# Optimization experiments

Hardware: AMD Instinct MI355X
Metric: run time of the kernel (lower is better)

## Reference

```python
import jax, jax.numpy as jnp
import numpy as np

B, N, D, H, C = 16, 196, 768, 3072, 10

def setup_inputs() -> dict:
    key = jax.random.key(0)
    ks = jax.random.split(key, 8)
    s1 = 1.0 / np.sqrt(D)
    s2 = 1.0 / np.sqrt(H)
    return {
        "x": jax.random.normal(ks[0], (B, N, D), jnp.float32),
        "y": jax.random.randint(ks[1], (B,), 0, C),
        "W1": jax.random.normal(ks[2], (H, D), jnp.float32) * s1,
        "b1": jax.random.normal(ks[3], (H,), jnp.float32) * 0.01,
        "W2": jax.random.normal(ks[4], (D, H), jnp.float32) * s2,
        "b2": jax.random.normal(ks[5], (D,), jnp.float32) * 0.01,
        "mask_fc1": jax.random.uniform(ks[6], (C, H, D), jnp.float32),
        "mask_fc2": jax.random.uniform(ks[7], (C, D, H), jnp.float32),
    }

def reference(x, y, W1, b1, W2, b2, mask_fc1, mask_fc2):
    # per-sample masked weights: [B, out, in]
    Wm1 = W1[None, :, :] * mask_fc1[y]          # [B, H, D]
    h = jnp.einsum('bni,boi->bno', x, Wm1) + b1  # [B, N, H]
    h = jax.nn.gelu(h, approximate=False)        # act (drop1/norm are identity)
    Wm2 = W2[None, :, :] * mask_fc2[y]           # [B, D, H]
    out = jnp.einsum('bni,boi->bno', h, Wm2) + b2  # [B, N, D]
    return out
```

## Files before the change

### kernel.cpp

```cpp
#include <hip/hip_runtime.h>
#include <hip/hip_bf16.h>
#include <math.h>

#define B_ 16
#define N_ 196
#define D_ 768
#define H_ 3072
#define C_ 10

typedef __attribute__((ext_vector_type(8))) short bf16x8;
typedef __attribute__((ext_vector_type(4))) float f32x4;

__device__ __forceinline__ ushort f2bu(float f) {
    union { float f; unsigned u; } c; c.f = f;
    unsigned u = c.u;
    unsigned r = (u + 0x7FFFu + ((u >> 16) & 1u)) >> 16;
    return (ushort)r;
}

__device__ __forceinline__ void gl_lds16(const ushort* g, ushort* l) {
    __builtin_amdgcn_global_load_lds(
        (const __attribute__((address_space(1))) void*)g,
        (__attribute__((address_space(3))) void*)l, 16, 0, 0);
}

__global__ void scan_y(const int* __restrict__ y, int* __restrict__ used) {
    if (threadIdx.x < C_) used[threadIdx.x] = 0;
    __syncthreads();
    if (threadIdx.x < B_) used[y[threadIdx.x]] = 1;
}

__global__ __launch_bounds__(256) void build_wm(
    const float* __restrict__ W, const float* __restrict__ mask,
    const int* __restrict__ used, ushort* __restrict__ outw)
{
    const int c = blockIdx.y;
    if (!used[c]) return;
    const long n = (long)H_ * D_;
    const long i = ((long)blockIdx.x * 256 + threadIdx.x) * 8;
    const float4* wp = reinterpret_cast<const float4*>(W + i);
    const float4* mp = reinterpret_cast<const float4*>(mask + c * n + i);
    float4 w0 = wp[0], w1 = wp[1], m0 = mp[0], m1 = mp[1];
    ushort t[8] = { f2bu(w0.x*m0.x), f2bu(w0.y*m0.y), f2bu(w0.z*m0.z), f2bu(w0.w*m0.w),
                    f2bu(w1.x*m1.x), f2bu(w1.y*m1.y), f2bu(w1.z*m1.z), f2bu(w1.w*m1.w) };
    *reinterpret_cast<uint4*>(outw + c * n + i) = *reinterpret_cast<const uint4*>(t);
}

__global__ __launch_bounds__(256) void cvt_x(const float* __restrict__ x,
                                             ushort* __restrict__ xb) {
    const int i = blockIdx.x * 256 + threadIdx.x;
    const float4* src = reinterpret_cast<const float4*>(x) + (size_t)i * 2;
    float4 a = src[0], b = src[1];
    ushort t[8] = { f2bu(a.x), f2bu(a.y), f2bu(a.z), f2bu(a.w),
                    f2bu(b.x), f2bu(b.y), f2bu(b.z), f2bu(b.w) };
    reinterpret_cast<uint4*>(xb)[i] = *reinterpret_cast<const uint4*>(t);
}

template<int EPI>
__global__ __launch_bounds__(256) void mgemm(
    const ushort* __restrict__ A0, const ushort* __restrict__ Wm,
    const int* __restrict__ y, const float* __restrict__ bias1,
    ushort* __restrict__ hout, float* __restrict__ pout)
{
    constexpr int K = (EPI == 0) ? D_ : H_;
    __shared__ ushort As[128][64];
    __shared__ ushort Bs[128][64];

    const int ot = blockIdx.x;
    const int mt = blockIdx.y;
    const int z  = blockIdx.z;
    const int b  = (EPI == 0) ? z : (z >> 2);
    const int sk = (EPI == 0) ? 0 : (z & 3);
    const int cls = y[b];
    const int tid = threadIdx.x, lane = tid & 63, wid = tid >> 6;
    const int wm = wid >> 1, wn = wid & 1;
    const int fr = lane & 15, fq = lane >> 4;
    const int lr = lane >> 3, le = (lane & 7) * 8;

    const ushort* Ab = A0 + (long)b * N_ * K;
    const ushort* Bb = Wm + (long)cls * ((long)H_ * D_) + (long)(ot * 128) * K;

    f32x4 acc[4][4] = {};
    const int kt0 = (EPI == 0) ? 0 : sk * 12;

    #pragma unroll
    for (int t = 0; t < 12; ++t) {
        const int k0 = (kt0 + t) * 64;
        #pragma unroll
        for (int i = 0; i < 4; ++i) {
            const int r = wid * 32 + i * 8;
            const int gm = min(mt * 128 + r + lr, N_ - 1);
            gl_lds16(Ab + (long)gm * K + k0 + le, &As[r][0]);
        }
        #pragma unroll
        for (int i = 0; i < 4; ++i) {
            const int r = wid * 32 + i * 8;
            gl_lds16(Bb + (long)(r + lr) * K + k0 + le, &Bs[r][0]);
        }
        __syncthreads();
        #pragma unroll
        for (int kk = 0; kk < 64; kk += 32) {
            bf16x8 af[4], bf[4];
            #pragma unroll
            for (int i = 0; i < 4; ++i)
                af[i] = *reinterpret_cast<const bf16x8*>(&As[wm*64 + i*16 + fr][kk + fq*8]);
            #pragma unroll
            for (int j = 0; j < 4; ++j)
                bf[j] = *reinterpret_cast<const bf16x8*>(&Bs[wn*64 + j*16 + fr][kk + fq*8]);
            #pragma unroll
            for (int i = 0; i < 4; ++i)
                #pragma unroll
                for (int j = 0; j < 4; ++j)
                    acc[i][j] = __builtin_amdgcn_mfma_f32_16x16x32_bf16(af[i], bf[j], acc[i][j], 0, 0, 0);
        }
        __syncthreads();
    }

    if (EPI == 0) {
        #pragma unroll
        for (int j = 0; j < 4; ++j) {
            const int o = ot*128 + wn*64 + j*16 + fr;
            const float bias = bias1[o];
            #pragma unroll
            for (int i = 0; i < 4; ++i) {
                #pragma unroll
                for (int e = 0; e < 4; ++e) {
                    const int m = mt*128 + wm*64 + i*16 + fq*4 + e;
                    if (m < N_) {
                        float v = acc[i][j][e] + bias;
                        v = 0.5f * v * (1.0f + erff(v * 0.70710678118654752f));
                        hout[((long)b * N_ + m) * H_ + o] = f2bu(v);
                    }
                }
            }
        }
    } else {
        float* op = pout + (size_t)sk * (size_t)(B_ * N_ * D_);
        #pragma unroll
        for (int j = 0; j < 4; ++j) {
            const int o = ot*128 + wn*64 + j*16 + fr;
            #pragma unroll
            for (int i = 0; i < 4; ++i) {
                #pragma unroll
                for (int e = 0; e < 4; ++e) {
                    const int m = mt*128 + wm*64 + i*16 + fq*4 + e;
                    if (m < N_)
                        op[((long)b * N_ + m) * D_ + o] = acc[i][j][e];
                }
            }
        }
    }
}

__global__ __launch_bounds__(256) void reduce_k(const float* __restrict__ part,
                                                const float* __restrict__ b2,
                                                float* __restrict__ out, int SK)
{
    const int i = blockIdx.x * 256 + threadIdx.x;
    const int stride4 = B_ * N_ * D_ / 4;
    float4 s = reinterpret_cast<const float4*>(part)[i];
    for (int k = 1; k < SK; ++k) {
        float4 p = reinterpret_cast<const float4*>(part)[(size_t)k * stride4 + i];
        s.x += p.x; s.y += p.y; s.z += p.z; s.w += p.w;
    }
    const int ob = (i % (D_ / 4)) * 4;
    float4 bias = *reinterpret_cast<const float4*>(b2 + ob);
    s.x += bias.x; s.y += bias.y; s.z += bias.z; s.w += bias.w;
    reinterpret_cast<float4*>(out)[i] = s;
}

__global__ __launch_bounds__(256) void fb_gemm1(
    const float* __restrict__ x, const int* __restrict__ y,
    const float* __restrict__ W1, const float* __restrict__ b1,
    const float* __restrict__ mask1, ushort* __restrict__ h)
{
    __shared__ ushort As[128][72];
    __shared__ ushort Bs[64][72];
    const int ot = blockIdx.x, mt = blockIdx.y, b = blockIdx.z;
    const int cls = y[b];
    const int tid = threadIdx.x, lane = tid & 63, wid = tid >> 6;
    const int wm = wid >> 1, wn = wid & 1;
    const int fr = lane & 15, fq = lane >> 4;
    const int sr = tid >> 2, sc = (tid & 3) * 16;
    f32x4 acc[4][2] = {};
    const long xbase = ((long)b * N_) * D_;
    const long wbase = (long)(ot * 64) * D_;
    const long mbase = ((long)cls * H_ + ot * 64) * D_;
    for (int kt = 0; kt < D_ / 64; ++kt) {
        const int k0 = kt * 64 + sc;
        #pragma unroll
        for (int half = 0; half < 2; ++half) {
            const int r = sr + half * 64;
            const int m = mt * 128 + r;
            ushort tmp[16];
            if (m < N_) {
                const float4* src = reinterpret_cast<const float4*>(x + xbase + (long)m * D_ + k0);
                #pragma unroll
                for (int j = 0; j < 4; ++j) {
                    float4 v = src[j];
                    tmp[4*j+0]=f2bu(v.x); tmp[4*j+1]=f2bu(v.y); tmp[4*j+2]=f2bu(v.z); tmp[4*j+3]=f2bu(v.w);
                }
            } else { for (int j = 0; j < 16; ++j) tmp[j] = 0; }
            *reinterpret_cast<uint4*>(&As[r][sc])   = *reinterpret_cast<const uint4*>(&tmp[0]);
            *reinterpret_cast<uint4*>(&As[r][sc+8]) = *reinterpret_cast<const uint4*>(&tmp[8]);
        }
        {
            const float4* wsrc = reinterpret_cast<const float4*>(W1 + wbase + (long)sr * D_ + k0);
            const float4* msrc = reinterpret_cast<const float4*>(mask1 + mbase + (long)sr * D_ + k0);
            ushort tmp[16];
            #pragma unroll
            for (int j = 0; j < 4; ++j) {
                float4 wv = wsrc[j], mv = msrc[j];
                tmp[4*j+0]=f2bu(wv.x*mv.x); tmp[4*j+1]=f2bu(wv.y*mv.y);
                tmp[4*j+2]=f2bu(wv.z*mv.z); tmp[4*j+3]=f2bu(wv.w*mv.w);
            }
            *reinterpret_cast<uint4*>(&Bs[sr][sc])   = *reinterpret_cast<const uint4*>(&tmp[0]);
            *reinterpret_cast<uint4*>(&Bs[sr][sc+8]) = *reinterpret_cast<const uint4*>(&tmp[8]);
        }
        __syncthreads();
        #pragma unroll
        for (int kk = 0; kk < 64; kk += 32) {
            bf16x8 af[4], bf[2];
            #pragma unroll
            for (int i = 0; i < 4; ++i) af[i] = *reinterpret_cast<const bf16x8*>(&As[wm*64+i*16+fr][kk+fq*8]);
            #pragma unroll
            for (int j = 0; j < 2; ++j) bf[j] = *reinterpret_cast<const bf16x8*>(&Bs[wn*32+j*16+fr][kk+fq*8]);
            #pragma unroll
            for (int i = 0; i < 4; ++i)
                #pragma unroll
                for (int j = 0; j < 2; ++j)
                    acc[i][j] = __builtin_amdgcn_mfma_f32_16x16x32_bf16(af[i], bf[j], acc[i][j], 0, 0, 0);
        }
        __syncthreads();
    }
    #pragma unroll
    for (int j = 0; j < 2; ++j) {
        const int o = ot*64 + wn*32 + j*16 + fr;
        const float bias = b1[o];
        #pragma unroll
        for (int i = 0; i < 4; ++i)
            #pragma unroll
            for (int e = 0; e < 4; ++e) {
                const int m = mt*128 + wm*64 + i*16 + fq*4 + e;
                if (m < N_) {
                    float v = acc[i][j][e] + bias;
                    v = 0.5f * v * (1.0f + erff(v * 0.70710678118654752f));
                    h[(((long)b * N_) + m) * H_ + o] = f2bu(v);
                }
            }
    }
}

__global__ __launch_bounds__(256) void fb_gemm2(
    const ushort* __restrict__ h, const int* __restrict__ y,
    const float* __restrict__ W2, const float* __restrict__ b2,
    const float* __restrict__ mask2, float* __restrict__ dst,
    int split, int nkt, int add_bias)
{
    __shared__ ushort As[128][72];
    __shared__ ushort Bs[64][72];
    const int ot = blockIdx.x, mt = blockIdx.y, z = blockIdx.z;
    const int b = z / split, sk = z - b * split;
    const int cls = y[b];
    const int tid = threadIdx.x, lane = tid & 63, wid = tid >> 6;
    const int wm = wid >> 1, wn = wid & 1;
    const int fr = lane & 15, fq = lane >> 4;
    const int sr = tid >> 2, sc = (tid & 3) * 16;
    f32x4 acc[4][2] = {};
    const long hbase = ((long)b * N_) * H_;
    const long wbase = (long)(ot * 64) * H_;
    const long mbase = ((long)cls * D_ + ot * 64) * H_;
    const int kt0 = sk * nkt;
    for (int kt = kt0; kt < kt0 + nkt; ++kt) {
        const int k0 = kt * 64 + sc;
        #pragma unroll
        for (int half = 0; half < 2; ++half) {
            const int r = sr + half * 64;
            const int m = mt * 128 + r;
            if (m < N_) {
                const uint4* src = reinterpret_cast<const uint4*>(h + hbase + (long)m * H_ + k0);
                *reinterpret_cast<uint4*>(&As[r][sc])   = src[0];
                *reinterpret_cast<uint4*>(&As[r][sc+8]) = src[1];
            } else {
                uint4 z4 = {0u,0u,0u,0u};
                *reinterpret_cast<uint4*>(&As[r][sc])   = z4;
                *reinterpret_cast<uint4*>(&As[r][sc+8]) = z4;
            }
        }
        {
            const float4* wsrc = reinterpret_cast<const float4*>(W2 + wbase + (long)sr * H_ + k0);
            const float4* msrc = reinterpret_cast<const float4*>(mask2 + mbase + (long)sr * H_ + k0);
            ushort tmp[16];
            #pragma unroll
            for (int j = 0; j < 4; ++j) {
                float4 wv = wsrc[j], mv = msrc[j];
                tmp[4*j+0]=f2bu(wv.x*mv.x); tmp[4*j+1]=f2bu(wv.y*mv.y);
                tmp[4*j+2]=f2bu(wv.z*mv.z); tmp[4*j+3]=f2bu(wv.w*mv.w);
            }
            *reinterpret_cast<uint4*>(&Bs[sr][sc])   = *reinterpret_cast<const uint4*>(&tmp[0]);
            *reinterpret_cast<uint4*>(&Bs[sr][sc+8]) = *reinterpret_cast<const uint4*>(&tmp[8]);
        }
        __syncthreads();
        #pragma unroll
        for (int kk = 0; kk < 64; kk += 32) {
            bf16x8 af[4], bf[2];
            #pragma unroll
            for (int i = 0; i < 4; ++i) af[i] = *reinterpret_cast<const bf16x8*>(&As[wm*64+i*16+fr][kk+fq*8]);
            #pragma unroll
            for (int j = 0; j < 2; ++j) bf[j] = *reinterpret_cast<const bf16x8*>(&Bs[wn*32+j*16+fr][kk+fq*8]);
            #pragma unroll
            for (int i = 0; i < 4; ++i)
                #pragma unroll
                for (int j = 0; j < 2; ++j)
                    acc[i][j] = __builtin_amdgcn_mfma_f32_16x16x32_bf16(af[i], bf[j], acc[i][j], 0, 0, 0);
        }
        __syncthreads();
    }
    float* op = dst + (size_t)sk * (size_t)(B_ * N_ * D_);
    #pragma unroll
    for (int j = 0; j < 2; ++j) {
        const int o = ot*64 + wn*32 + j*16 + fr;
        const float bias = add_bias ? b2[o] : 0.0f;
        #pragma unroll
        for (int i = 0; i < 4; ++i)
            #pragma unroll
            for (int e = 0; e < 4; ++e) {
                const int m = mt*128 + wm*64 + i*16 + fq*4 + e;
                if (m < N_) op[(((long)b * N_) + m) * D_ + o] = acc[i][j][e] + bias;
            }
    }
}

extern "C" void kernel_launch(void* const* d_in, const int* in_sizes, int n_in,
                              void* d_out, int out_size, void* d_ws, size_t ws_size,
                              hipStream_t stream) {
    const float* x  = (const float*)d_in[0];
    const int*   y  = (const int*)d_in[1];
    const float* W1 = (const float*)d_in[2];
    const float* b1 = (const float*)d_in[3];
    const float* W2 = (const float*)d_in[4];
    const float* b2 = (const float*)d_in[5];
    const float* m1 = (const float*)d_in[6];
    const float* m2 = (const float*)d_in[7];
    float* out = (float*)d_out;

    const size_t hB  = (size_t)B_ * N_ * H_ * 2;
    const size_t oB  = (size_t)B_ * N_ * D_ * 4;
    const size_t xB  = (size_t)B_ * N_ * D_ * 2;
    const size_t wmB = (size_t)C_ * H_ * D_ * 2;

    const size_t off_part = hB;
    const size_t off_xb   = hB + 4 * oB;
    const size_t off_used = off_xb + xB;
    const size_t off_wm1  = off_used + 256;
    const size_t off_wm2  = off_wm1 + wmB;
    const size_t need     = off_wm2 + wmB;

    ushort* h = (ushort*)d_ws;

    if (ws_size >= need) {
        float*  part = (float*)((char*)d_ws + off_part);
        ushort* xb   = (ushort*)((char*)d_ws + off_xb);
        int*    used = (int*)((char*)d_ws + off_used);
        ushort* wm1  = (ushort*)((char*)d_ws + off_wm1);
        ushort* wm2  = (ushort*)((char*)d_ws + off_wm2);

        scan_y<<<1, 64, 0, stream>>>(y, used);
        build_wm<<<dim3(1152, C_), 256, 0, stream>>>(W1, m1, used, wm1);
        build_wm<<<dim3(1152, C_), 256, 0, stream>>>(W2, m2, used, wm2);
        cvt_x<<<1176, 256, 0, stream>>>(x, xb);
        mgemm<0><<<dim3(24, 2, 16), 256, 0, stream>>>(xb, wm1, y, b1, h, nullptr);
        mgemm<1><<<dim3(6, 2, 64), 256, 0, stream>>>(h, wm2, y, nullptr, nullptr, part);
        reduce_k<<<(B_ * N_ * D_ / 4) / 256, 256, 0, stream>>>(part, b2, out, 4);
    } else {
        int SK = 0;
        if      (ws_size >= hB + 4 * oB) SK = 4;
        else if (ws_size >= hB + 2 * oB) SK = 2;
        float* part = (float*)((char*)d_ws + hB);
        dim3 g1(H_ / 64, 2, B_);
        fb_gemm1<<<g1, 256, 0, stream>>>(x, y, W1, b1, m1, h);
        if (SK) {
            dim3 g2(D_ / 64, 2, B_ * SK);
            fb_gemm2<<<g2, 256, 0, stream>>>(h, y, W2, b2, m2, part, SK, 48 / SK, 0);
            reduce_k<<<(B_ * N_ * D_ / 4) / 256, 256, 0, stream>>>(part, b2, out, SK);
        } else {
            dim3 g2(D_ / 64, 2, B_);
            fb_gemm2<<<g2, 256, 0, stream>>>(h, y, W2, b2, m2, out, 1, 48, 1);
        }
    }
}
```

Baseline: 144.3 us.

## Fuse prep kernels and overlap fc1 GEMM with fc2 weight masking

Merges the scan, masked-W1 build and x conversion into one launch, then co-schedules the first GEMM with the masked-W2 build in a single heterogeneous grid so the W2 build overlaps GEMM1. Each block now checks y itself instead of reading a separate used-flag array. Activations are padded to 256 rows per batch, which removes the row clamp and the bounds checks in the GEMM loads and epilogue. In exchange GEMM1 computes GELU on padded garbage rows, and the combined grid mixes compute-bound and memory-bound blocks whose scheduling order is not controlled.

After: 142.1 us. Within noise of the previous version (-1.5%).

```diff
diff --git a/kernel.cpp b/kernel.cpp
--- a/kernel.cpp
+++ b/kernel.cpp
@@ -7,6 +7,7 @@
 #define D_ 768
 #define H_ 3072
 #define C_ 10
+#define MPAD 256
 
 typedef __attribute__((ext_vector_type(8))) short bf16x8;
 typedef __attribute__((ext_vector_type(4))) float f32x4;
@@ -24,60 +25,43 @@
         (__attribute__((address_space(3))) void*)l, 16, 0, 0);
 }
 
-__global__ void scan_y(const int* __restrict__ y, int* __restrict__ used) {
-    if (threadIdx.x < C_) used[threadIdx.x] = 0;
-    __syncthreads();
-    if (threadIdx.x < B_) used[y[threadIdx.x]] = 1;
-}
-
-__global__ __launch_bounds__(256) void build_wm(
+__device__ __forceinline__ void build_wm_chunk(
     const float* __restrict__ W, const float* __restrict__ mask,
-    const int* __restrict__ used, ushort* __restrict__ outw)
-{
-    const int c = blockIdx.y;
-    if (!used[c]) return;
+    const int* __restrict__ y, ushort* __restrict__ outw,
+    int c, int chunk)
+{
+    bool used = false;
+    #pragma unroll
+    for (int t = 0; t < B_; ++t) used |= (y[t] == c);
+    if (!used) return;
     const long n = (long)H_ * D_;
-    const long i = ((long)blockIdx.x * 256 + threadIdx.x) * 8;
+    const long i = (long)chunk * 2048 + threadIdx.x * 8;
     const float4* wp = reinterpret_cast<const float4*>(W + i);
     const float4* mp = reinterpret_cast<const float4*>(mask + c * n + i);
     float4 w0 = wp[0], w1 = wp[1], m0 = mp[0], m1 = mp[1];
-    ushort t[8] = { f2bu(w0.x*m0.x), f2bu(w0.y*m0.y), f2bu(w0.z*m0.z), f2bu(w0.w*m0.w),
-                    f2bu(w1.x*m1.x), f2bu(w1.y*m1.y), f2bu(w1.z*m1.z), f2bu(w1.w*m1.w) };
-    *reinterpret_cast<uint4*>(outw + c * n + i) = *reinterpret_cast<const uint4*>(t);
-}
-
-__global__ __launch_bounds__(256) void cvt_x(const float* __restrict__ x,
-                                             ushort* __restrict__ xb) {
-    const int i = blockIdx.x * 256 + threadIdx.x;
-    const float4* src = reinterpret_cast<const float4*>(x) + (size_t)i * 2;
-    float4 a = src[0], b = src[1];
-    ushort t[8] = { f2bu(a.x), f2bu(a.y), f2bu(a.z), f2bu(a.w),
-                    f2bu(b.x), f2bu(b.y), f2bu(b.z), f2bu(b.w) };
-    reinterpret_cast<uint4*>(xb)[i] = *reinterpret_cast<const uint4*>(t);
+    ushort t8[8] = { f2bu(w0.x*m0.x), f2bu(w0.y*m0.y), f2bu(w0.z*m0.z), f2bu(w0.w*m0.w),
+                     f2bu(w1.x*m1.x), f2bu(w1.y*m1.y), f2bu(w1.z*m1.z), f2bu(w1.w*m1.w) };
+    *reinterpret_cast<uint4*>(outw + c * n + i) = *reinterpret_cast<const uint4*>(t8);
 }
 
 template<int EPI>
-__global__ __launch_bounds__(256) void mgemm(
+__device__ __forceinline__ void gemm_core(
     const ushort* __restrict__ A0, const ushort* __restrict__ Wm,
     const int* __restrict__ y, const float* __restrict__ bias1,
-    ushort* __restrict__ hout, float* __restrict__ pout)
+    ushort* __restrict__ hout, float* __restrict__ pout,
+    int ot, int mt, int b, int sk)
 {
     constexpr int K = (EPI == 0) ? D_ : H_;
     __shared__ ushort As[128][64];
     __shared__ ushort Bs[128][64];
 
-    const int ot = blockIdx.x;
-    const int mt = blockIdx.y;
-    const int z  = blockIdx.z;
-    const int b  = (EPI == 0) ? z : (z >> 2);
-    const int sk = (EPI == 0) ? 0 : (z & 3);
     const int cls = y[b];
     const int tid = threadIdx.x, lane = tid & 63, wid = tid >> 6;
     const int wm = wid >> 1, wn = wid & 1;
     const int fr = lane & 15, fq = lane >> 4;
     const int lr = lane >> 3, le = (lane & 7) * 8;
 
-    const ushort* Ab = A0 + (long)b * N_ * K;
+    const ushort* Ab = A0 + ((long)b * MPAD + mt * 128) * K;
     const ushort* Bb = Wm + (long)cls * ((long)H_ * D_) + (long)(ot * 128) * K;
 
     f32x4 acc[4][4] = {};
@@ -89,8 +73,7 @@
         #pragma unroll
         for (int i = 0; i < 4; ++i) {
             const int r = wid * 32 + i * 8;
-            const int gm = min(mt * 128 + r + lr, N_ - 1);
-            gl_lds16(Ab + (long)gm * K + k0 + le, &As[r][0]);
+            gl_lds16(Ab + (long)(r + lr) * K + k0 + le, &As[r][0]);
         }
         #pragma unroll
         for (int i = 0; i < 4; ++i) {
@@ -126,11 +109,9 @@
                 #pragma unroll
                 for (int e = 0; e < 4; ++e) {
                     const int m = mt*128 + wm*64 + i*16 + fq*4 + e;
-                    if (m < N_) {
-                        float v = acc[i][j][e] + bias;
-                        v = 0.5f * v * (1.0f + erff(v * 0.70710678118654752f));
-                        hout[((long)b * N_ + m) * H_ + o] = f2bu(v);
-                    }
+                    float v = acc[i][j][e] + bias;
+                    v = 0.5f * v * (1.0f + erff(v * 0.70710678118654752f));
+                    hout[((long)b * MPAD + m) * H_ + o] = f2bu(v);
                 }
             }
         }
@@ -150,6 +131,53 @@
             }
         }
     }
+}
+
+__global__ __launch_bounds__(256) void prep1(
+    const float* __restrict__ x, const int* __restrict__ y,
+    const float* __restrict__ W1, const float* __restrict__ mask1,
+    ushort* __restrict__ xb, ushort* __restrict__ wm1)
+{
+    const int bid = blockIdx.x;
+    if (bid < 11520) {
+        build_wm_chunk(W1, mask1, y, wm1, bid / 1152, bid % 1152);
+    } else {
+        const int i = (bid - 11520) * 256 + threadIdx.x;
+        const int r = i / 96;
+        const int c8 = (i % 96) * 8;
+        const int b = r / 196, n = r - b * 196;
+        const float4* src = reinterpret_cast<const float4*>(x + (long)r * D_ + c8);
+        float4 a = src[0], bb = src[1];
+        ushort t[8] = { f2bu(a.x), f2bu(a.y), f2bu(a.z), f2bu(a.w),
+                        f2bu(bb.x), f2bu(bb.y), f2bu(bb.z), f2bu(bb.w) };
+        *reinterpret_cast<uint4*>(xb + ((long)b * MPAD + n) * D_ + c8) =
+            *reinterpret_cast<const uint4*>(t);
+    }
+}
+
+__global__ __launch_bounds__(256) void fat2(
+    const ushort* __restrict__ xb, const ushort* __restrict__ wm1,
+    const int* __restrict__ y, const float* __restrict__ b1,
+    ushort* __restrict__ h,
+    const float* __restrict__ W2, const float* __restrict__ mask2,
+    ushort* __restrict__ wm2)
+{
+    const int bid = blockIdx.x;
+    if (bid < 768) {
+        const int ot = bid % 24, mt = (bid / 24) & 1, b = bid / 48;
+        gemm_core<0>(xb, wm1, y, b1, h, nullptr, ot, mt, b, 0);
+    } else {
+        const int idx = bid - 768;
+        build_wm_chunk(W2, mask2, y, wm2, idx / 1152, idx % 1152);
+    }
+}
+
+__global__ __launch_bounds__(256) void mgemm2(
+    const ushort* __restrict__ h, const ushort* __restrict__ wm2,
+    const int* __restrict__ y, float* __restrict__ part)
+{
+    const int ot = blockIdx.x, mt = blockIdx.y, z = blockIdx.z;
+    gemm_core<1>(h, wm2, y, nullptr, nullptr, part, ot, mt, z >> 2, z & 3);
 }
 
 __global__ __launch_bounds__(256) void reduce_k(const float* __restrict__ part,
@@ -344,39 +372,36 @@
     const float* m2 = (const float*)d_in[7];
     float* out = (float*)d_out;
 
-    const size_t hB  = (size_t)B_ * N_ * H_ * 2;
-    const size_t oB  = (size_t)B_ * N_ * D_ * 4;
-    const size_t xB  = (size_t)B_ * N_ * D_ * 2;
-    const size_t wmB = (size_t)C_ * H_ * D_ * 2;
-
-    const size_t off_part = hB;
-    const size_t off_xb   = hB + 4 * oB;
-    const size_t off_used = off_xb + xB;
-    const size_t off_wm1  = off_used + 256;
+    const size_t xbB  = (size_t)B_ * MPAD * D_ * 2;
+    const size_t hB   = (size_t)B_ * MPAD * H_ * 2;
+    const size_t oB   = (size_t)B_ * N_ * D_ * 4;
+    const size_t wmB  = (size_t)C_ * H_ * D_ * 2;
+
+    const size_t off_xb   = 0;
+    const size_t off_h    = off_xb + xbB;
+    const size_t off_part = off_h + hB;
+    const size_t off_wm1  = off_part + 4 * oB;
     const size_t off_wm2  = off_wm1 + wmB;
     const size_t need     = off_wm2 + wmB;
 
-    ushort* h = (ushort*)d_ws;
-
     if (ws_size >= need) {
-        float*  part = (float*)((char*)d_ws + off_part);
-        ushort* xb   = (ushort*)((char*)d_ws + off_xb);
-        int*    used = (int*)((char*)d_ws + off_used);
-        ushort* wm1  = (ushort*)((char*)d_ws + off_wm1);
-        ushort* wm2  = (ushort*)((char*)d_ws + off_wm2);
-
-        scan_y<<<1, 64, 0, stream>>>(y, used);
-        build_wm<<<dim3(1152, C_), 256, 0, stream>>>(W1, m1, used, wm1);
-        build_wm<<<dim3(1152, C_), 256, 0, stream>>>(W2, m2, used, wm2);
-        cvt_x<<<1176, 256, 0, stream>>>(x, xb);
-        mgemm<0><<<dim3(24, 2, 16), 256, 0, stream>>>(xb, wm1, y, b1, h, nullptr);
-        mgemm<1><<<dim3(6, 2, 64), 256, 0, stream>>>(h, wm2, y, nullptr, nullptr, part);
+        ushort* xb  = (ushort*)((char*)d_ws + off_xb);
+        ushort* h   = (ushort*)((char*)d_ws + off_h);
+        float* part = (float*)((char*)d_ws + off_part);
+        ushort* wm1 = (ushort*)((char*)d_ws + off_wm1);
+        ushort* wm2 = (ushort*)((char*)d_ws + off_wm2);
+
+        prep1<<<11520 + 1176, 256, 0, stream>>>(x, y, W1, m1, xb, wm1);
+        fat2<<<768 + 11520, 256, 0, stream>>>(xb, wm1, y, b1, h, W2, m2, wm2);
+        mgemm2<<<dim3(6, 2, 64), 256, 0, stream>>>(h, wm2, y, part);
         reduce_k<<<(B_ * N_ * D_ / 4) / 256, 256, 0, stream>>>(part, b2, out, 4);
     } else {
+        const size_t fb_hB = (size_t)B_ * N_ * H_ * 2;
+        ushort* h = (ushort*)d_ws;
         int SK = 0;
-        if      (ws_size >= hB + 4 * oB) SK = 4;
-        else if (ws_size >= hB + 2 * oB) SK = 2;
-        float* part = (float*)((char*)d_ws + hB);
+        if      (ws_size >= fb_hB + 4 * oB) SK = 4;
+        else if (ws_size >= fb_hB + 2 * oB) SK = 2;
+        float* part = (float*)((char*)d_ws + fb_hB);
         dim3 g1(H_ / 64, 2, B_);
         fb_gemm1<<<g1, 256, 0, stream>>>(x, y, W1, b1, m1, h);
         if (SK) {
```
